# Kernel optimization log

Hardware: AMD Instinct MI355X
Metric: run time of the kernel (lower is better)

The kernel has to match this reference:

```python
import jax, jax.numpy as jnp
import numpy as np

B, D, L = 8, 512, 2000          # batch, encoder_out_dim, seq_len
E = 300                          # embedding_dim
N1, N2 = 118, 8929               # hierarchy level sizes


def setup_inputs() -> dict:
    key = jax.random.key(0)
    k = jax.random.split(key, 6)
    H = jax.random.normal(k[0], (B, D, L), dtype=jnp.float32)
    Q1w = jax.random.normal(k[1], (N1, E), dtype=jnp.float32) * 0.05   # cat_embedding_matrix
    Q2w = jax.random.normal(k[2], (N2, E), dtype=jnp.float32) * 0.05   # label_embedding_matrix
    # Q12: xavier_uniform over [N2, N1]
    bound = float(np.sqrt(6.0 / (N1 + N2)))
    Q12w = jax.random.uniform(k[3], (N2, N1), minval=-bound, maxval=bound, dtype=jnp.float32)
    # 1x1 conv mapping: weight [D, E], bias [D] (kernel_size=1 squeezed)
    cbound = float(np.sqrt(1.0 / E))
    Wmap = jax.random.uniform(k[4], (D, E), minval=-cbound, maxval=cbound, dtype=jnp.float32)
    bmap = jax.random.uniform(k[5], (D,), minval=-cbound, maxval=cbound, dtype=jnp.float32)
    return {"H": H, "Q1w": Q1w, "Q2w": Q2w, "Q12w": Q12w, "Wmap": Wmap, "bmap": bmap}


def reference(H, Q1w, Q2w, Q12w, Wmap, bmap):
    # 1x1 conv mapping == affine map over embedding dim: [n, E] @ [E, D] + b
    Q1 = Q1w @ Wmap.T + bmap                      # [N1, D]
    E1 = jnp.einsum('nd,bdl->bnl', Q1, H)         # level-1 scores [B, N1, L]
    A1 = jax.nn.softmax(E1, axis=2)
    C1 = jnp.einsum('bnl,bdl->bnd', A1, H)        # [B, N1, D]
    C1 = jnp.einsum('mn,bnd->bmd', Q12w, C1)      # project to level 2: [B, N2, D]
    Q2 = (Q2w @ Wmap.T + bmap) * C1               # [N2, D] * [B, N2, D]
    E2 = jnp.einsum('bmd,bdl->bml', Q2, H)        # level-2 scores [B, N2, L]
    A2 = jax.nn.softmax(E2, axis=2)
    C2 = jnp.einsum('bml,bdl->bmd', A2, H)        # [B, N2, D]
    return (C2, A2)
```

## Files before the change

### kernel.cpp

```cpp
#include <hip/hip_runtime.h>

typedef short    bf16x8 __attribute__((ext_vector_type(8)));
typedef float    f32x4  __attribute__((ext_vector_type(4)));
typedef unsigned short u16x8 __attribute__((ext_vector_type(8)));

__device__ __forceinline__ unsigned short f2bf(float f) {
    unsigned u = __float_as_uint(f);
    return (unsigned short)((u + 0x7fffu + ((u >> 16) & 1u)) >> 16);
}
__device__ __forceinline__ float bf2f(unsigned short h) {
    return __uint_as_float((unsigned)h << 16);
}

template<bool> struct otype            { using T = float; };
template<>     struct otype<true>      { using T = unsigned short; };

template<int BM,int BN,int TM,int TN,bool BT,bool VA,bool VB,bool OB>
__launch_bounds__(256)
__global__ void gemm_f32(const float* __restrict__ A, int lda, long long sA,
                         const float* __restrict__ B, int ldb, long long sB,
                         void* __restrict__ Cv, int ldc, long long sC,
                         int M, int N, int K,
                         const float* __restrict__ bias,
                         const float* __restrict__ mul, int mulld)
{
    constexpr int BK  = 16;
    constexpr int GSA = BM*4/TM;
    constexpr int GSB = BN*4/TN;
    __shared__ float As[BK][BM+4];
    __shared__ float Bs[BK][BN+4];

    const int bz = blockIdx.z;
    A += (long long)bz * sA;
    B += (long long)bz * sB;
    using OT = typename otype<OB>::T;
    OT* C = (OT*)Cv + (long long)bz * sC;
    const int m0 = blockIdx.y * BM;
    const int n0 = blockIdx.x * BN;
    const int tid = threadIdx.x;
    const int tm = tid >> 4;
    const int tn = tid & 15;

    float acc[TM][TN];
#pragma unroll
    for (int i=0;i<TM;++i)
#pragma unroll
        for (int j=0;j<TN;++j) acc[i][j]=0.f;

    for (int k0=0;k0<K;k0+=BK) {
        if constexpr (VA) {
#pragma unroll
            for (int r=0;r<BM*BK/1024;++r) {
                int v = tid + r*256;
                int m = v >> 2, k4 = (v & 3)*4;
                int gm = m0+m, gk = k0+k4;
                float4 val = make_float4(0.f,0.f,0.f,0.f);
                if (gm < M) {
                    if (gk+3 < K) {
                        val = *reinterpret_cast<const float4*>(A + (long long)gm*lda + gk);
                    } else {
                        float t0 = (gk   < K) ? A[(long long)gm*lda+gk  ] : 0.f;
                        float t1 = (gk+1 < K) ? A[(long long)gm*lda+gk+1] : 0.f;
                        float t2 = (gk+2 < K) ? A[(long long)gm*lda+gk+2] : 0.f;
                        val = make_float4(t0,t1,t2,0.f);
                    }
                }
                As[k4+0][m]=val.x; As[k4+1][m]=val.y; As[k4+2][m]=val.z; As[k4+3][m]=val.w;
            }
        } else {
#pragma unroll
            for (int r=0;r<BM*BK/256;++r) {
                int e = tid + r*256;
                int m = e >> 4, k = e & 15;
                int gm=m0+m, gk=k0+k;
                As[k][m] = (gm<M && gk<K) ? A[(long long)gm*lda+gk] : 0.f;
            }
        }
        if constexpr (!BT) {
            if constexpr (VB) {
#pragma unroll
                for (int r=0;r<BK*BN/1024;++r) {
                    int v = tid + r*256;
                    int k = v / (BN/4), n4 = (v % (BN/4))*4;
                    int gk=k0+k, gn=n0+n4;
                    float4 val = make_float4(0.f,0.f,0.f,0.f);
                    if (gk < K) {
                        if (gn+3 < N) {
                            val = *reinterpret_cast<const float4*>(B + (long long)gk*ldb + gn);
                        } else {
                            float t0=(gn  <N)?B[(long long)gk*ldb+gn  ]:0.f;
                            float t1=(gn+1<N)?B[(long long)gk*ldb+gn+1]:0.f;
                            float t2=(gn+2<N)?B[(long long)gk*ldb+gn+2]:0.f;
                            val = make_float4(t0,t1,t2,0.f);
                        }
                    }
                    Bs[k][n4+0]=val.x; Bs[k][n4+1]=val.y; Bs[k][n4+2]=val.z; Bs[k][n4+3]=val.w;
                }
            } else {
#pragma unroll
                for (int r=0;r<BK*BN/256;++r) {
                    int e = tid + r*256;
                    int k = e / BN, n = e % BN;
                    int gk=k0+k, gn=n0+n;
                    Bs[k][n] = (gk<K && gn<N) ? B[(long long)gk*ldb+gn] : 0.f;
                }
            }
        } else {
            if constexpr (VB) {
#pragma unroll
                for (int r=0;r<BN*BK/1024;++r) {
                    int v = tid + r*256;
                    int n = v >> 2, k4 = (v&3)*4;
                    int gn=n0+n, gk=k0+k4;
                    float4 val = make_float4(0.f,0.f,0.f,0.f);
                    if (gn < N) {
                        if (gk+3 < K) {
                            val = *reinterpret_cast<const float4*>(B + (long long)gn*ldb + gk);
                        } else {
                            float t0=(gk  <K)?B[(long long)gn*ldb+gk  ]:0.f;
                            float t1=(gk+1<K)?B[(long long)gn*ldb+gk+1]:0.f;
                            float t2=(gk+2<K)?B[(long long)gn*ldb+gk+2]:0.f;
                            val=make_float4(t0,t1,t2,0.f);
                        }
                    }
                    Bs[k4+0][n]=val.x; Bs[k4+1][n]=val.y; Bs[k4+2][n]=val.z; Bs[k4+3][n]=val.w;
                }
            } else {
#pragma unroll
                for (int r=0;r<BN*BK/256;++r) {
                    int e = tid + r*256;
                    int n = e >> 4, k = e & 15;
                    int gn=n0+n, gk=k0+k;
                    Bs[k][n] = (gn<N && gk<K) ? B[(long long)gn*ldb+gk] : 0.f;
                }
            }
        }
        __syncthreads();
#pragma unroll
        for (int kk=0;kk<BK;++kk) {
            float a[TM], bb[TN];
#pragma unroll
            for (int g=0;g<TM/4;++g) {
                float4 t = *reinterpret_cast<const float4*>(&As[kk][g*GSA + tm*4]);
                a[4*g+0]=t.x; a[4*g+1]=t.y; a[4*g+2]=t.z; a[4*g+3]=t.w;
            }
#pragma unroll
            for (int g=0;g<TN/4;++g) {
                float4 t = *reinterpret_cast<const float4*>(&Bs[kk][g*GSB + tn*4]);
                bb[4*g+0]=t.x; bb[4*g+1]=t.y; bb[4*g+2]=t.z; bb[4*g+3]=t.w;
            }
#pragma unroll
            for (int i=0;i<TM;++i)
#pragma unroll
                for (int j=0;j<TN;++j)
                    acc[i][j] = fmaf(a[i], bb[j], acc[i][j]);
        }
        __syncthreads();
    }
#pragma unroll
    for (int i=0;i<TM;++i) {
        int row = m0 + (i>>2)*GSA + tm*4 + (i&3);
        if (row < M) {
#pragma unroll
            for (int j=0;j<TN;++j) {
                int col = n0 + (j>>2)*GSB + tn*4 + (j&3);
                if (col < N) {
                    float val = acc[i][j];
                    if (bias) val += bias[col];
                    if (mul)  val *= mul[(long long)row*mulld + col];
                    if constexpr (OB) C[(long long)row*ldc + col] = f2bf(val);
                    else              C[(long long)row*ldc + col] = val;
                }
            }
        }
    }
}

template<unsigned F>
__launch_bounds__(512, 4)
__global__ void gemm_mfma_p(const unsigned short* __restrict__ A, int lda, long long sA,
                            const unsigned short* __restrict__ Bt, int ldb, long long sB,
                            void* __restrict__ Cv, int ldc, long long sC,
                            int M, int Ncols, int NX, int NY, int NT,
                            const float* __restrict__ bias,
                            const float* __restrict__ mul, int ldm,
                            float* __restrict__ partial, long long pstride,
                            const float* __restrict__ hsum,
                            const float* __restrict__ invs)
{
    __shared__ unsigned short lds[3][12288];

    const int nwg = gridDim.x;
    const int q = nwg >> 3, r = nwg & 7;
    const int xcd = blockIdx.x & 7, idx = blockIdx.x >> 3;
    const int wg = (xcd < r ? xcd*(q+1) : r*(q+1) + (xcd-r)*q) + idx;
    const int nx = wg % NX;
    const int t1 = wg / NX;
    const int my = t1 % NY;
    const int bz = t1 / NY;

    const int tid  = threadIdx.x;
    const int lane = tid & 63, wid = tid >> 6;
    const int wr = wid >> 2, wc = wid & 3;
    const int fr = lane & 15, fq = lane >> 4;
    const int m0 = my * 128;
    const int n0 = nx * 256;

    A  += (long long)bz * sA;
    Bt += (long long)bz * sB;

    const int srow = tid >> 2;
    const int scz  = (tid & 3) ^ ((srow >> 1) & 3);
    long long arow = m0 + srow; if (arow > M-1) arow = M-1;
    const unsigned short* aSrc  = A  + arow*lda + scz*8;
    const unsigned short* bSrc0 = Bt + (long long)(n0 + srow)*ldb + scz*8;
    const unsigned short* bSrc1 = bSrc0 + 128ll*ldb;

    int aoff[4], boff[4];
#pragma unroll
    for (int m=0;m<4;++m) {
        const int ra = wr*64 + m*16 + fr;
        aoff[m] = ra*64 + ((fq ^ ((ra>>1)&3))*16);
    }
#pragma unroll
    for (int n=0;n<4;++n) {
        const int rb = wc*64 + n*16 + fr;
        boff[n] = 8192 + rb*64 + ((fq ^ ((rb>>1)&3))*16);
    }

    f32x4 acc[4][4];
#pragma unroll
    for (int i=0;i<4;++i)
#pragma unroll
        for (int j=0;j<4;++j) acc[i][j] = (f32x4)(0.f);

    auto stage = [&](int s, int t) {
        const int koff = t*32;
        char* base = (char*)&lds[s][0];
        __builtin_amdgcn_global_load_lds(
            (const __attribute__((address_space(1))) void*)(aSrc + koff),
            (__attribute__((address_space(3))) void*)(base + tid*16), 16, 0, 0);
        __builtin_amdgcn_global_load_lds(
            (const __attribute__((address_space(1))) void*)(bSrc0 + koff),
            (__attribute__((address_space(3))) void*)(base + 8192 + tid*16), 16, 0, 0);
        __builtin_amdgcn_global_load_lds(
            (const __attribute__((address_space(1))) void*)(bSrc1 + koff),
            (__attribute__((address_space(3))) void*)(base + 16384 + tid*16), 16, 0, 0);
    };

    stage(0, 0);
    stage(1, NT > 1 ? 1 : 0);
    asm volatile("s_waitcnt vmcnt(3)" ::: "memory");
    __builtin_amdgcn_s_barrier();

    int cur = 0, stg = 2;
    for (int kt = 0; kt < NT; ++kt) {
        int tnx = kt + 2; if (tnx > NT-1) tnx = NT-1;
        stage(stg, tnx);
        const char* bp = (const char*)&lds[cur][0];
        bf16x8 a[4], b[4];
#pragma unroll
        for (int m=0;m<4;++m) a[m] = *(const bf16x8*)(bp + aoff[m]);
#pragma unroll
        for (int n=0;n<4;++n) b[n] = *(const bf16x8*)(bp + boff[n]);
        __builtin_amdgcn_s_setprio(1);
#pragma unroll
        for (int m=0;m<4;++m)
#pragma unroll
            for (int n=0;n<4;++n)
                acc[m][n] = __builtin_amdgcn_mfma_f32_16x16x32_bf16(a[m], b[n], acc[m][n], 0, 0, 0);
        __builtin_amdgcn_s_setprio(0);
        asm volatile("s_waitcnt lgkmcnt(0)" ::: "memory");
        asm volatile("s_waitcnt vmcnt(3)" ::: "memory");
        __builtin_amdgcn_s_barrier();
        cur = (cur == 2) ? 0 : cur + 1;
        stg = (stg == 2) ? 0 : stg + 1;
    }

    if constexpr ((F & 16) != 0) {
        __shared__ float sp[4][128];
        unsigned short* Cb = (unsigned short*)Cv + (long long)bz * sC;
        float rp[4][4];
#pragma unroll
        for (int m=0;m<4;++m)
#pragma unroll
            for (int j=0;j<4;++j) rp[m][j] = 0.f;
#pragma unroll
        for (int m=0;m<4;++m) {
            const int rb = m0 + wr*64 + m*16 + fq*4;
#pragma unroll
            for (int n=0;n<4;++n) {
                const int col = n0 + wc*64 + n*16 + fr;
#pragma unroll
                for (int j=0;j<4;++j) {
                    float x = __expf(acc[m][n][j]) - 1.0f;
                    rp[m][j] += x;
                    const int row = rb + j;
                    if (row < M) Cb[(long long)row*ldc + col] = f2bf(x);
                }
            }
        }
#pragma unroll
        for (int m=0;m<4;++m)
#pragma unroll
            for (int j=0;j<4;++j) {
                float s = rp[m][j];
                s += __shfl_xor(s, 1); s += __shfl_xor(s, 2);
                s += __shfl_xor(s, 4); s += __shfl_xor(s, 8);
                rp[m][j] = s;
            }
        if (fr == 0) {
#pragma unroll
            for (int m=0;m<4;++m)
#pragma unroll
                for (int j=0;j<4;++j)
                    sp[wc][wr*64 + m*16 + fq*4 + j] = rp[m][j];
        }
        __syncthreads();
        if (tid < 128) {
            const int row = m0 + tid;
            if (row < M) {
                float s = sp[0][tid] + sp[1][tid] + sp[2][tid] + sp[3][tid];
                partial[(long long)nx*pstride + (long long)bz*M + row] = s;
            }
        }
    } else if constexpr ((F & 8) != 0) {
        unsigned short* Ct = (unsigned short*)Cv + (long long)bz * sC;
#pragma unroll
        for (int m=0;m<4;++m) {
            const int rb = m0 + wr*64 + m*16 + fq*4;
#pragma unroll
            for (int n=0;n<4;++n) {
                const int col = n0 + wc*64 + n*16 + fr;
                if (col < Ncols) {
#pragma unroll
                    for (int j=0;j<4;++j) {
                        const int row = rb + j;
                        float val = (row < M) ? acc[m][n][j] : 0.f;
                        Ct[(long long)col*ldc + row] = f2bf(val);
                    }
                }
            }
        }
    } else {
        float*          Cf = (float*)Cv + (long long)bz * sC;
        unsigned short* Cb = (unsigned short*)Cv + (long long)bz * sC;
#pragma unroll
        for (int m=0;m<4;++m) {
            const int rb = m0 + wr*64 + m*16 + fq*4;
#pragma unroll
            for (int n=0;n<4;++n) {
                const int col = n0 + wc*64 + n*16 + fr;
                if (col < Ncols) {
                    float bv = 0.f, hv = 0.f;
                    if constexpr ((F & 1) != 0) bv = bias[col];
                    if constexpr ((F & 32) != 0) hv = hsum[(long long)bz*Ncols + col];
#pragma unroll
                    for (int j=0;j<4;++j) {
                        const int row = rb + j;
                        if (row < M) {
                            float val = acc[m][n][j];
                            if constexpr ((F & 1) != 0)  val += bv;
                            if constexpr ((F & 2) != 0)  val *= mul[(long long)row*ldm + col];
                            if constexpr ((F & 32) != 0) val = (val + hv) * invs[(long long)bz*M + row];
                            if constexpr ((F & 4) != 0)  Cb[(long long)row*ldc + col] = f2bf(val);
                            else                         Cf[(long long)row*ldc + col] = val;
                        }
                    }
                }
            }
        }
    }
}

template<bool AF32>
__launch_bounds__(512, 2)
__global__ void gemm_mfma(const void* __restrict__ Ain, int lda, long long sA,
                          const unsigned short* __restrict__ Bt, int ldb, long long sB,
                          float* __restrict__ C, int ldc, long long sC,
                          int M, int N, int K, int NT)
{
    __shared__ unsigned short As[2][128*32];
    __shared__ unsigned short Bs[2][256*32];

    const int tid  = threadIdx.x;
    const int lane = tid & 63, wid = tid >> 6;
    const int wr = wid >> 2, wc = wid & 3;
    const int fr = lane & 15, fq = lane >> 4;
    const int bz = blockIdx.z;
    const int m0 = blockIdx.y * 128;
    const int n0 = blockIdx.x * 256;

    const unsigned short* Ab = nullptr;
    const float*          Af = nullptr;
    if constexpr (AF32) Af = (const float*)Ain + (long long)bz * sA;
    else                Ab = (const unsigned short*)Ain + (long long)bz * sA;
    Bt += (long long)bz * sB;
    C  += (long long)bz * sC;

    const int srow = tid >> 2;
    const int sc   = tid & 3;
    const int scz  = sc ^ ((srow >> 1) & 3);
    int arow = m0 + srow; if (arow > M-1) arow = M-1;
    const bool am_ok = (m0 + srow) < M;
    const long long brow0 = n0 + srow;
    const long long brow1 = n0 + 128 + srow;
    const int ldsA  = wid << 10;
    const int ldsB0 = wid << 10;
    const int ldsB1 = 8192 + (wid << 10);

    f32x4 acc[4][4];
#pragma unroll
    for (int i=0;i<4;++i)
#pragma unroll
        for (int j=0;j<4;++j) acc[i][j] = (f32x4)(0.f);

    auto stage = [&](int buf, int t) {
        const long long koff = (long long)t * 32;
        __builtin_amdgcn_global_load_lds(
            (const __attribute__((address_space(1))) void*)(Bt + brow0*ldb + koff + scz*8),
            (__attribute__((address_space(3))) void*)((char*)&Bs[buf][0] + ldsB0), 16, 0, 0);
        __builtin_amdgcn_global_load_lds(
            (const __attribute__((address_space(1))) void*)(Bt + brow1*ldb + koff + scz*8),
            (__attribute__((address_space(3))) void*)((char*)&Bs[buf][0] + ldsB1), 16, 0, 0);
        if constexpr (!AF32) {
            __builtin_amdgcn_global_load_lds(
                (const __attribute__((address_space(1))) void*)(Ab + (long long)arow*lda + koff + scz*8),
                (__attribute__((address_space(3))) void*)((char*)&As[buf][0] + ldsA), 16, 0, 0);
        } else {
            const float* src = Af + (long long)arow*lda + koff + scz*8;
            const int kk = t*32 + scz*8;
            float4 z = make_float4(0.f,0.f,0.f,0.f);
            float4 v0 = (am_ok && kk   < K) ? *(const float4*)(src  ) : z;
            float4 v1 = (am_ok && kk+4 < K) ? *(const float4*)(src+4) : z;
            u16x8 o;
            o[0]=f2bf(v0.x); o[1]=f2bf(v0.y); o[2]=f2bf(v0.z); o[3]=f2bf(v0.w);
            o[4]=f2bf(v1.x); o[5]=f2bf(v1.y); o[6]=f2bf(v1.z); o[7]=f2bf(v1.w);
            *(u16x8*)((char*)&As[buf][0] + tid*16) = o;
        }
    };

    stage(0, 0);
    int cur = 0;
    for (int t = 0; t < NT; ++t) {
        __syncthreads();
        if (t + 1 < NT) stage(cur ^ 1, t + 1);
        const unsigned short* as = As[cur];
        const unsigned short* bs = Bs[cur];
        bf16x8 a[4], b[4];
#pragma unroll
        for (int m=0;m<4;++m) {
            const int ra = wr*64 + m*16 + fr;
            a[m] = *(const bf16x8*)(as + ra*32 + (fq ^ ((ra>>1)&3))*8);
        }
#pragma unroll
        for (int n=0;n<4;++n) {
            const int rb = wc*64 + n*16 + fr;
            b[n] = *(const bf16x8*)(bs + rb*32 + (fq ^ ((rb>>1)&3))*8);
        }
        __builtin_amdgcn_s_setprio(1);
#pragma unroll
        for (int m=0;m<4;++m)
#pragma unroll
            for (int n=0;n<4;++n)
                acc[m][n] = __builtin_amdgcn_mfma_f32_16x16x32_bf16(a[m], b[n], acc[m][n], 0, 0, 0);
        __builtin_amdgcn_s_setprio(0);
        cur ^= 1;
    }
#pragma unroll
    for (int m=0;m<4;++m) {
        const int rb = m0 + wr*64 + m*16 + fq*4;
#pragma unroll
        for (int n=0;n<4;++n) {
            const int col = n0 + wc*64 + n*16 + fr;
            if (col < N) {
#pragma unroll
                for (int j=0;j<4;++j) {
                    const int row = rb + j;
                    if (row < M) C[(long long)row*ldc + col] = acc[m][n][j];
                }
            }
        }
    }
}

__global__ __launch_bounds__(256) void cvt_pad_bf16(const float* __restrict__ H,
                                                    unsigned short* __restrict__ Hb)
{
    const long long idx = (long long)blockIdx.x * 256 + threadIdx.x;
    const long long row = idx >> 8;
    const int l0 = (int)(idx & 255) * 8;
    u16x8 o = (u16x8)(unsigned short)0;
    if (l0 + 8 <= 2000) {
        const float* s = H + row*2000 + l0;
        float4 v0 = *(const float4*)(s);
        float4 v1 = *(const float4*)(s+4);
        o[0]=f2bf(v0.x); o[1]=f2bf(v0.y); o[2]=f2bf(v0.z); o[3]=f2bf(v0.w);
        o[4]=f2bf(v1.x); o[5]=f2bf(v1.y); o[6]=f2bf(v1.z); o[7]=f2bf(v1.w);
    }
    *(u16x8*)(Hb + row*2048 + l0) = o;
}

__global__ __launch_bounds__(256) void cvt_transpose_bf16(const float* __restrict__ H,
                                                          unsigned short* __restrict__ Ht)
{
    __shared__ unsigned short T[64][80];
    const int bz = blockIdx.z;
    const int d0 = blockIdx.y * 64;
    const int l0 = blockIdx.x * 64;
    const float* Hsrc = H + ((long long)bz*512 + d0) * 2000;
    unsigned short* Hdst = Ht + ((long long)bz*2048 + l0) * 512 + d0;
    const int tid = threadIdx.x;
    const int dl = tid >> 2;
    const int lc = (tid & 3) * 16;
#pragma unroll
    for (int i=0;i<4;++i) {
        const int l = lc + i*4;
        const int gl = l0 + l;
        float4 v = make_float4(0.f,0.f,0.f,0.f);
        if (gl < 2000) v = *(const float4*)(Hsrc + (long long)dl*2000 + gl);
        T[l+0][dl] = f2bf(v.x);
        T[l+1][dl] = f2bf(v.y);
        T[l+2][dl] = f2bf(v.z);
        T[l+3][dl] = f2bf(v.w);
    }
    __syncthreads();
    const int ll = tid >> 2;
    const int dc = (tid & 3) * 16;
    u16x8 w0 = *(const u16x8*)&T[ll][dc];
    u16x8 w1 = *(const u16x8*)&T[ll][dc+8];
    *(u16x8*)(Hdst + (long long)ll*512 + dc    ) = w0;
    *(u16x8*)(Hdst + (long long)ll*512 + dc + 8) = w1;
}

__global__ __launch_bounds__(256) void cvt_rows_bf16(const float* __restrict__ src,
                                                     unsigned short* __restrict__ dst,
                                                     long long rows, int scols, int dcols)
{
    const long long i = (long long)blockIdx.x * 256 + threadIdx.x;
    if (i < rows * (long long)dcols) {
        const long long r = i / dcols;
        const int c = (int)(i - r*dcols);
        dst[i] = (c < scols) ? f2bf(src[r*scols + c]) : (unsigned short)0;
    }
}

__global__ __launch_bounds__(256) void hsum_k(const float* __restrict__ H,
                                              float* __restrict__ Hsum)
{
    const int row  = blockIdx.x*4 + (threadIdx.x >> 6);
    const int lane = threadIdx.x & 63;
    const float* h = H + (long long)row * 2000;
    float s = 0.f;
    for (int c = lane*4; c < 2000; c += 256) {
        float4 v = *(const float4*)(h + c);
        s += (v.x + v.y) + (v.z + v.w);
    }
#pragma unroll
    for (int o=32;o;o>>=1) s += __shfl_xor(s, o);
    if (lane == 0) Hsum[row] = s;
}

__global__ __launch_bounds__(256) void normalize_k(const unsigned short* __restrict__ A2b,
                                                   const float* __restrict__ partial,
                                                   long long pstride,
                                                   float* __restrict__ A2,
                                                   float* __restrict__ invs)
{
    const long long row = blockIdx.x;
    float s = 0.f;
#pragma unroll
    for (int i=0;i<8;++i) s += partial[i*pstride + row];
    const float inv = 1.0f / (2000.0f + s);
    if (threadIdx.x == 0) invs[row] = inv;
    const int tid = threadIdx.x;
    if (tid < 250) {
        u16x8 v = *(const u16x8*)(A2b + row*2048 + tid*8);
        float* a2 = A2 + row*2000 + tid*8;
        float4 o0, o1;
        o0.x = (1.0f + bf2f((unsigned short)v[0])) * inv;
        o0.y = (1.0f + bf2f((unsigned short)v[1])) * inv;
        o0.z = (1.0f + bf2f((unsigned short)v[2])) * inv;
        o0.w = (1.0f + bf2f((unsigned short)v[3])) * inv;
        o1.x = (1.0f + bf2f((unsigned short)v[4])) * inv;
        o1.y = (1.0f + bf2f((unsigned short)v[5])) * inv;
        o1.z = (1.0f + bf2f((unsigned short)v[6])) * inv;
        o1.w = (1.0f + bf2f((unsigned short)v[7])) * inv;
        *(float4*)(a2    ) = o0;
        *(float4*)(a2 + 4) = o1;
    }
}

__global__ __launch_bounds__(256) void softmax_rows(float* __restrict__ X, int L,
                                                    unsigned short* __restrict__ Xb, int Lb)
{
    const long long row = blockIdx.x;
    float* x = X + row * (long long)L;
    const int tid = threadIdx.x;
    const int nv = L >> 2;
    const bool h0 = tid < nv;
    const bool h1 = tid + 256 < nv;
    float4 t0 = make_float4(0.f,0.f,0.f,0.f);
    float4 t1 = make_float4(0.f,0.f,0.f,0.f);
    float mx = -3.402823e38f;
    if (h0) { t0 = *reinterpret_cast<const float4*>(x + 4*tid);
              mx = fmaxf(fmaxf(t0.x,t0.y), fmaxf(t0.z,t0.w)); }
    if (h1) { t1 = *reinterpret_cast<const float4*>(x + 4*(tid+256));
              mx = fmaxf(mx, fmaxf(fmaxf(t1.x,t1.y), fmaxf(t1.z,t1.w))); }
    __shared__ float sred[4];
#pragma unroll
    for (int o=32;o;o>>=1) mx = fmaxf(mx, __shfl_xor(mx, o));
    if ((tid & 63)==0) sred[tid>>6] = mx;
    __syncthreads();
    mx = fmaxf(fmaxf(sred[0],sred[1]), fmaxf(sred[2],sred[3]));
    __syncthreads();
    float s = 0.f;
    if (h0) {
        t0.x=__expf(t0.x-mx); t0.y=__expf(t0.y-mx); t0.z=__expf(t0.z-mx); t0.w=__expf(t0.w-mx);
        s += (t0.x+t0.y)+(t0.z+t0.w);
    }
    if (h1) {
        t1.x=__expf(t1.x-mx); t1.y=__expf(t1.y-mx); t1.z=__expf(t1.z-mx); t1.w=__expf(t1.w-mx);
        s += (t1.x+t1.y)+(t1.z+t1.w);
    }
#pragma unroll
    for (int o=32;o;o>>=1) s += __shfl_xor(s, o);
    if ((tid & 63)==0) sred[tid>>6] = s;
    __syncthreads();
    s = (sred[0]+sred[1])+(sred[2]+sred[3]);
    const float inv = 1.0f / s;
    if (h0) { t0.x*=inv; t0.y*=inv; t0.z*=inv; t0.w*=inv;
              *reinterpret_cast<float4*>(x + 4*tid) = t0; }
    if (h1) { t1.x*=inv; t1.y*=inv; t1.z*=inv; t1.w*=inv;
              *reinterpret_cast<float4*>(x + 4*(tid+256)) = t1; }
    if (Xb) {
        unsigned short* xb = Xb + row * (long long)Lb;
        if (h0) {
            ushort4 o; o.x=f2bf(t0.x); o.y=f2bf(t0.y); o.z=f2bf(t0.z); o.w=f2bf(t0.w);
            *reinterpret_cast<ushort4*>(xb + 4*tid) = o;
        }
        if (h1) {
            ushort4 o; o.x=f2bf(t1.x); o.y=f2bf(t1.y); o.z=f2bf(t1.z); o.w=f2bf(t1.w);
            *reinterpret_cast<ushort4*>(xb + 4*(tid+256)) = o;
        }
        if (tid < (Lb - L)/4) {
            ushort4 z; z.x=z.y=z.z=z.w=0;
            *reinterpret_cast<ushort4*>(xb + L + 4*tid) = z;
        }
    }
}

extern "C" void kernel_launch(void* const* d_in, const int* in_sizes, int n_in,
                              void* d_out, int out_size, void* d_ws, size_t ws_size,
                              hipStream_t stream)
{
    const float* H    = (const float*)d_in[0];
    const float* Q1w  = (const float*)d_in[1];
    const float* Q2w  = (const float*)d_in[2];
    const float* Q12w = (const float*)d_in[3];
    const float* Wmap = (const float*)d_in[4];
    const float* bmap = (const float*)d_in[5];

    constexpr long long B=8, D=512, L=2000, N1=118, N2=8929;
    constexpr long long C2E = B*N2*D;
    float* out = (float*)d_out;
    float* C2  = out;
    float* A2  = out + C2E;

    dim3 blk(256);

    size_t off = 0;
    auto alloc = [&](size_t n)->size_t { off = (off + 255) & ~(size_t)255; size_t o = off; off += n; return o; };
    const size_t oHb    = alloc(8ll*512*2048*2);
    const size_t oHtb   = alloc(8ll*2048*512*2);
    const size_t oWb    = alloc(512ll*320*2);
    const size_t oQ1wb  = alloc(118ll*320*2);
    const size_t oQ2wb  = alloc(8929ll*320*2);
    const size_t oQ12wb = alloc(8929ll*128*2);
    const size_t oQ1b   = alloc(118ll*512*2);
    const size_t oEmb   = alloc(8929ll*512*4);
    const size_t oE1    = alloc(8ll*118*2000*4);
    const size_t oA1b   = alloc(8ll*118*2048*2);
    const size_t oC1tb  = alloc(8ll*512*128*2);
    const size_t oQ2b   = alloc(8ll*8929*512*2);
    const size_t oA2b   = alloc(8ll*8929*2048*2);
    const size_t oPart  = alloc(8ll*8*8929*4);
    const size_t oInvs  = alloc(8ll*8929*4);
    const size_t oHsum  = alloc(8ll*512*4);
    const size_t FULL_NEED = off;

    char* ws = (char*)d_ws;

    if (ws_size >= FULL_NEED) {
        unsigned short* Hb    = (unsigned short*)(ws + oHb);
        unsigned short* Htb   = (unsigned short*)(ws + oHtb);
        unsigned short* Wb    = (unsigned short*)(ws + oWb);
        unsigned short* Q1wb  = (unsigned short*)(ws + oQ1wb);
        unsigned short* Q2wb  = (unsigned short*)(ws + oQ2wb);
        unsigned short* Q12wb = (unsigned short*)(ws + oQ12wb);
        unsigned short* Q1b   = (unsigned short*)(ws + oQ1b);
        float*          emb   = (float*)(ws + oEmb);
        float*          E1    = (float*)(ws + oE1);
        unsigned short* A1b   = (unsigned short*)(ws + oA1b);
        unsigned short* C1tb  = (unsigned short*)(ws + oC1tb);
        unsigned short* Q2b   = (unsigned short*)(ws + oQ2b);
        unsigned short* A2b   = (unsigned short*)(ws + oA2b);
        float*          part  = (float*)(ws + oPart);
        float*          invs  = (float*)(ws + oInvs);
        float*          Hsum  = (float*)(ws + oHsum);

        cvt_pad_bf16<<<dim3(4096), blk, 0, stream>>>(H, Hb);
        cvt_transpose_bf16<<<dim3(32,8,8), blk, 0, stream>>>(H, Htb);
        cvt_rows_bf16<<<dim3((512*320+255)/256), blk, 0, stream>>>(Wmap, Wb, 512, 300, 320);
        cvt_rows_bf16<<<dim3((118*320+255)/256), blk, 0, stream>>>(Q1w, Q1wb, 118, 300, 320);
        cvt_rows_bf16<<<dim3((8929*320+255)/256), blk, 0, stream>>>(Q2w, Q2wb, 8929, 300, 320);
        cvt_rows_bf16<<<dim3((8929*128+255)/256), blk, 0, stream>>>(Q12w, Q12wb, 8929, 118, 128);
        hsum_k<<<dim3(1024), blk, 0, stream>>>(H, Hsum);

        gemm_mfma_p<5><<<dim3(2), dim3(512), 0, stream>>>(
            Q1wb, 320, 0, Wb, 320, 0, Q1b, 512, 0, 118, 512, 2, 1, 10,
            bmap, nullptr, 0, nullptr, 0, nullptr, nullptr);
        gemm_mfma_p<1><<<dim3(140), dim3(512), 0, stream>>>(
            Q2wb, 320, 0, Wb, 320, 0, emb, 512, 0, 8929, 512, 2, 70, 10,
            bmap, nullptr, 0, nullptr, 0, nullptr, nullptr);
        gemm_mfma_p<0><<<dim3(64), dim3(512), 0, stream>>>(
            Q1b, 512, 0, Htb, 512, 2048*512, E1, 2000, N1*L, 118, 2000, 8, 1, 16,
            nullptr, nullptr, 0, nullptr, 0, nullptr, nullptr);
        softmax_rows<<<dim3((unsigned)(B*N1)), blk, 0, stream>>>(E1, 2000, A1b, 2048);
        gemm_mfma_p<12><<<dim3(16), dim3(512), 0, stream>>>(
            A1b, 2048, N1*2048, Hb, 2048, 512*2048, C1tb, 128, 512*128, 118, 512, 2, 1, 64,
            nullptr, nullptr, 0, nullptr, 0, nullptr, nullptr);
        gemm_mfma_p<6><<<dim3(1120), dim3(512), 0, stream>>>(
            Q12wb, 128, 0, C1tb, 128, 512*128, Q2b, 512, N2*D, 8929, 512, 2, 70, 4,
            nullptr, emb, 512, nullptr, 0, nullptr, nullptr);
        gemm_mfma_p<16><<<dim3(4480), dim3(512), 0, stream>>>(
            Q2b, 512, N2*D, Htb, 512, 2048*512, A2b, 2048, N2*2048, 8929, 2048, 8, 70, 16,
            nullptr, nullptr, 0, part, 8ll*8929, nullptr, nullptr);
        normalize_k<<<dim3((unsigned)(B*N2)), blk, 0, stream>>>(A2b, part, 8ll*8929, A2, invs);
        gemm_mfma_p<32><<<dim3(1120), dim3(512), 0, stream>>>(
            A2b, 2048, N2*2048, Hb, 2048, 512*2048, C2, 512, N2*D, 8929, 512, 2, 70, 64,
            nullptr, nullptr, 0, nullptr, 0, Hsum, invs);
        return;
    }

    float* Q1  = A2;
    float* emb = Q1  + N1*D;
    float* E1  = emb + N2*D;
    float* C1  = E1  + B*N1*L;

    gemm_f32<64,64,4,4,true,true,true,false><<<dim3(8,2,1), blk, 0, stream>>>(
        Q1w, 300, 0, Wmap, 300, 0, Q1, 512, 0, (int)N1, (int)D, 300, bmap, nullptr, 0);
    gemm_f32<64,64,4,4,true,true,true,false><<<dim3(8,140,1), blk, 0, stream>>>(
        Q2w, 300, 0, Wmap, 300, 0, emb, 512, 0, (int)N2, (int)D, 300, bmap, nullptr, 0);
    gemm_f32<64,64,4,4,false,true,true,false><<<dim3(32,2,8), blk, 0, stream>>>(
        Q1, 512, 0, H, 2000, D*L, E1, 2000, N1*L, (int)N1, (int)L, (int)D, nullptr, nullptr, 0);
    softmax_rows<<<dim3((unsigned)(B*N1)), blk, 0, stream>>>(E1, (int)L, nullptr, 0);
    gemm_f32<64,64,4,4,true,true,true,false><<<dim3(8,2,8), blk, 0, stream>>>(
        E1, 2000, N1*L, H, 2000, D*L, C1, 512, N1*D, (int)N1, (int)D, (int)L, nullptr, nullptr, 0);

    constexpr long long HBE = 8ll*512*2048;
    if (ws_size >= (size_t)(2*HBE*sizeof(unsigned short))) {
        unsigned short* Hb  = (unsigned short*)d_ws;
        unsigned short* Htb = Hb + HBE;
        cvt_pad_bf16<<<dim3(4096), blk, 0, stream>>>(H, Hb);
        cvt_transpose_bf16<<<dim3(32,8,8), blk, 0, stream>>>(H, Htb);
        unsigned short* Q2b = (unsigned short*)C2;
        gemm_f32<64,64,4,4,false,false,true,true><<<dim3(8,140,8), blk, 0, stream>>>(
            Q12w, 118, 0, C1, 512, N1*D, Q2b, 512, N2*D, (int)N2, (int)D, (int)N1, nullptr, emb, 512);
        gemm_mfma_p<0><<<dim3(4480), dim3(512), 0, stream>>>(
            Q2b, 512, N2*D, Htb, 512, 2048*512, A2, 2000, N2*L, (int)N2, (int)L, 8, 70, 16,
            nullptr, nullptr, 0, nullptr, 0, nullptr, nullptr);
        softmax_rows<<<dim3((unsigned)(B*N2)), blk, 0, stream>>>(A2, (int)L, nullptr, 0);
        gemm_mfma<true><<<dim3(2,70,8), dim3(512), 0, stream>>>(
            A2, 2000, N2*L, Hb, 2048, 512*2048, C2, 512, N2*D,
            (int)N2, (int)D, 2000, 63);
    } else {
        float* Q2 = C2;
        gemm_f32<64,64,4,4,false,false,true,false><<<dim3(8,140,8), blk, 0, stream>>>(
            Q12w, 118, 0, C1, 512, N1*D, Q2, 512, N2*D, (int)N2, (int)D, (int)N1, nullptr, emb, 512);
        gemm_f32<128,128,8,8,false,true,true,false><<<dim3(16,70,8), blk, 0, stream>>>(
            Q2, 512, N2*D, H, 2000, D*L, A2, 2000, N2*L, (int)N2, (int)L, (int)D, nullptr, nullptr, 0);
        softmax_rows<<<dim3((unsigned)(B*N2)), blk, 0, stream>>>(A2, (int)L, nullptr, 0);
        gemm_f32<128,128,8,8,true,true,true,false><<<dim3(4,70,8), blk, 0, stream>>>(
            A2, 2000, N2*L, H, 2000, D*L, C2, 512, N2*D, (int)N2, (int)D, (int)L, nullptr, nullptr, 0);
    }
}
```

Before: 830.8 us.

## Fuse A2 normalization into final GEMM and merge H preprocessing kernels

Removes the separate normalize_k pass. The final A2·H GEMM now writes the normalized fp32 A2 from its staged LDS tiles (blocks with nx==0 only), with a small invs_k kernel computing the reciprocal row sums first. It also merges the pad, transpose and row-sum passes over H into one prep_h kernel plus a tiny reduction, so H is read once instead of three times. In exchange the GEMM carries extra global stores and a looser vmcnt wait in half its blocks, which may unbalance work across blocks.

```diff
diff --git a/kernel.cpp b/kernel.cpp
--- a/kernel.cpp
+++ b/kernel.cpp
@@ -186,7 +186,9 @@
                             const float* __restrict__ mul, int ldm,
                             float* __restrict__ partial, long long pstride,
                             const float* __restrict__ hsum,
-                            const float* __restrict__ invs)
+                            const float* __restrict__ invs,
+                            float* __restrict__ a2out,
+                            float* __restrict__ dump)
 {
     __shared__ unsigned short lds[3][12288];
 
@@ -215,6 +217,21 @@
     const unsigned short* aSrc  = A  + arow*lda + scz*8;
     const unsigned short* bSrc0 = Bt + (long long)(n0 + srow)*ldb + scz*8;
     const unsigned short* bSrc1 = bSrc0 + 128ll*ldb;
+
+    bool wrblk = false, a2ok = false;
+    float invv = 0.f;
+    float* a2p = nullptr;
+    if constexpr ((F & 64) != 0) {
+        wrblk = (nx == 0);
+        if (wrblk) {
+            const int rrow = m0 + srow;
+            a2ok = rrow < M;
+            const long long ridx = (long long)bz*M + (a2ok ? rrow : M-1);
+            invv = invs[ridx];
+            asm volatile("" : "+v"(invv));
+            a2p = a2out + ridx*2000ll;
+        }
+    }
 
     int aoff[4], boff[4];
 #pragma unroll
@@ -270,8 +287,32 @@
             for (int n=0;n<4;++n)
                 acc[m][n] = __builtin_amdgcn_mfma_f32_16x16x32_bf16(a[m], b[n], acc[m][n], 0, 0, 0);
         __builtin_amdgcn_s_setprio(0);
+        if constexpr ((F & 64) != 0) {
+            if (wrblk) {
+                u16x8 av = *(const u16x8*)(bp + (tid << 4));
+                const int col0 = kt*32 + scz*8;
+                const bool ok = a2ok && (col0 < 2000);
+                float* p0 = ok ? (a2p + col0) : (dump + (tid << 3));
+                float4 o0, o1;
+                o0.x = fmaf(bf2f((unsigned short)av[0]), invv, invv);
+                o0.y = fmaf(bf2f((unsigned short)av[1]), invv, invv);
+                o0.z = fmaf(bf2f((unsigned short)av[2]), invv, invv);
+                o0.w = fmaf(bf2f((unsigned short)av[3]), invv, invv);
+                o1.x = fmaf(bf2f((unsigned short)av[4]), invv, invv);
+                o1.y = fmaf(bf2f((unsigned short)av[5]), invv, invv);
+                o1.z = fmaf(bf2f((unsigned short)av[6]), invv, invv);
+                o1.w = fmaf(bf2f((unsigned short)av[7]), invv, invv);
+                *(float4*)(p0    ) = o0;
+                *(float4*)(p0 + 4) = o1;
+            }
+        }
         asm volatile("s_waitcnt lgkmcnt(0)" ::: "memory");
-        asm volatile("s_waitcnt vmcnt(3)" ::: "memory");
+        if constexpr ((F & 64) != 0) {
+            if (wrblk) asm volatile("s_waitcnt vmcnt(5)" ::: "memory");
+            else       asm volatile("s_waitcnt vmcnt(3)" ::: "memory");
+        } else {
+            asm volatile("s_waitcnt vmcnt(3)" ::: "memory");
+        }
         __builtin_amdgcn_s_barrier();
         cur = (cur == 2) ? 0 : cur + 1;
         stg = (stg == 2) ? 0 : stg + 1;
@@ -484,6 +525,79 @@
     }
 }
 
+__global__ __launch_bounds__(256) void prep_h(const float* __restrict__ H,
+                                              unsigned short* __restrict__ Hb,
+                                              unsigned short* __restrict__ Htb,
+                                              float* __restrict__ hpart)
+{
+    __shared__ unsigned short T[64][80];
+    const int bz = blockIdx.z;
+    const int d0 = blockIdx.y * 64;
+    const int l0 = blockIdx.x * 64;
+    const float* Hsrc = H + ((long long)bz*512 + d0) * 2000;
+    const int tid = threadIdx.x;
+    const int dl = tid >> 2;
+    const int lc = (tid & 3) * 16;
+    float4 v[4];
+    float s = 0.f;
+#pragma unroll
+    for (int i=0;i<4;++i) {
+        const int gl = l0 + lc + i*4;
+        v[i] = make_float4(0.f,0.f,0.f,0.f);
+        if (gl < 2000) v[i] = *(const float4*)(Hsrc + (long long)dl*2000 + gl);
+        s += (v[i].x + v[i].y) + (v[i].z + v[i].w);
+        T[lc+i*4+0][dl] = f2bf(v[i].x);
+        T[lc+i*4+1][dl] = f2bf(v[i].y);
+        T[lc+i*4+2][dl] = f2bf(v[i].z);
+        T[lc+i*4+3][dl] = f2bf(v[i].w);
+    }
+    {
+        unsigned short* hb = Hb + ((long long)bz*512 + d0 + dl)*2048 + l0 + lc;
+        u16x8 h0, h1;
+        h0[0]=f2bf(v[0].x); h0[1]=f2bf(v[0].y); h0[2]=f2bf(v[0].z); h0[3]=f2bf(v[0].w);
+        h0[4]=f2bf(v[1].x); h0[5]=f2bf(v[1].y); h0[6]=f2bf(v[1].z); h0[7]=f2bf(v[1].w);
+        h1[0]=f2bf(v[2].x); h1[1]=f2bf(v[2].y); h1[2]=f2bf(v[2].z); h1[3]=f2bf(v[2].w);
+        h1[4]=f2bf(v[3].x); h1[5]=f2bf(v[3].y); h1[6]=f2bf(v[3].z); h1[7]=f2bf(v[3].w);
+        *(u16x8*)(hb    ) = h0;
+        *(u16x8*)(hb + 8) = h1;
+    }
+    s += __shfl_xor(s, 1);
+    s += __shfl_xor(s, 2);
+    if ((tid & 3) == 0)
+        hpart[(long long)blockIdx.x*4096 + bz*512 + d0 + dl] = s;
+    __syncthreads();
+    unsigned short* Hdst = Htb + ((long long)bz*2048 + l0) * 512 + d0;
+    const int ll = tid >> 2;
+    const int dc = (tid & 3) * 16;
+    u16x8 w0 = *(const u16x8*)&T[ll][dc];
+    u16x8 w1 = *(const u16x8*)&T[ll][dc+8];
+    *(u16x8*)(Hdst + (long long)ll*512 + dc    ) = w0;
+    *(u16x8*)(Hdst + (long long)ll*512 + dc + 8) = w1;
+}
+
+__global__ __launch_bounds__(256) void reduce_hsum(const float* __restrict__ hpart,
+                                                   float* __restrict__ Hsum)
+{
+    const int r = blockIdx.x*256 + threadIdx.x;
+    float s = 0.f;
+#pragma unroll
+    for (int i=0;i<32;++i) s += hpart[(long long)i*4096 + r];
+    Hsum[r] = s;
+}
+
+__global__ __launch_bounds__(256) void invs_k(const float* __restrict__ partial,
+                                              long long pstride,
+                                              float* __restrict__ invs, int n)
+{
+    const int r = blockIdx.x*256 + threadIdx.x;
+    if (r < n) {
+        float s = 0.f;
+#pragma unroll
+        for (int i=0;i<8;++i) s += partial[i*pstride + r];
+        invs[r] = 1.0f / (2000.0f + s);
+    }
+}
+
 __global__ __launch_bounds__(256) void cvt_pad_bf16(const float* __restrict__ H,
                                                     unsigned short* __restrict__ Hb)
 {
@@ -542,52 +656,6 @@
         const long long r = i / dcols;
         const int c = (int)(i - r*dcols);
         dst[i] = (c < scols) ? f2bf(src[r*scols + c]) : (unsigned short)0;
-    }
-}
-
-__global__ __launch_bounds__(256) void hsum_k(const float* __restrict__ H,
-                                              float* __restrict__ Hsum)
-{
-    const int row  = blockIdx.x*4 + (threadIdx.x >> 6);
-    const int lane = threadIdx.x & 63;
-    const float* h = H + (long long)row * 2000;
-    float s = 0.f;
-    for (int c = lane*4; c < 2000; c += 256) {
-        float4 v = *(const float4*)(h + c);
-        s += (v.x + v.y) + (v.z + v.w);
-    }
-#pragma unroll
-    for (int o=32;o;o>>=1) s += __shfl_xor(s, o);
-    if (lane == 0) Hsum[row] = s;
-}
-
-__global__ __launch_bounds__(256) void normalize_k(const unsigned short* __restrict__ A2b,
-                                                   const float* __restrict__ partial,
-                                                   long long pstride,
-                                                   float* __restrict__ A2,
-                                                   float* __restrict__ invs)
-{
-    const long long row = blockIdx.x;
-    float s = 0.f;
-#pragma unroll
-    for (int i=0;i<8;++i) s += partial[i*pstride + row];
-    const float inv = 1.0f / (2000.0f + s);
-    if (threadIdx.x == 0) invs[row] = inv;
-    const int tid = threadIdx.x;
-    if (tid < 250) {
-        u16x8 v = *(const u16x8*)(A2b + row*2048 + tid*8);
-        float* a2 = A2 + row*2000 + tid*8;
-        float4 o0, o1;
-        o0.x = (1.0f + bf2f((unsigned short)v[0])) * inv;
-        o0.y = (1.0f + bf2f((unsigned short)v[1])) * inv;
-        o0.z = (1.0f + bf2f((unsigned short)v[2])) * inv;
-        o0.w = (1.0f + bf2f((unsigned short)v[3])) * inv;
-        o1.x = (1.0f + bf2f((unsigned short)v[4])) * inv;
-        o1.y = (1.0f + bf2f((unsigned short)v[5])) * inv;
-        o1.z = (1.0f + bf2f((unsigned short)v[6])) * inv;
-        o1.w = (1.0f + bf2f((unsigned short)v[7])) * inv;
-        *(float4*)(a2    ) = o0;
-        *(float4*)(a2 + 4) = o1;
     }
 }
 
@@ -687,6 +755,7 @@
     const size_t oPart  = alloc(8ll*8*8929*4);
     const size_t oInvs  = alloc(8ll*8929*4);
     const size_t oHsum  = alloc(8ll*512*4);
+    const size_t oHpart = alloc(32ll*4096*4);
     const size_t FULL_NEED = off;
 
     char* ws = (char*)d_ws;
@@ -708,38 +777,38 @@
         float*          part  = (float*)(ws + oPart);
         float*          invs  = (float*)(ws + oInvs);
         float*          Hsum  = (float*)(ws + oHsum);
-
-        cvt_pad_bf16<<<dim3(4096), blk, 0, stream>>>(H, Hb);
-        cvt_transpose_bf16<<<dim3(32,8,8), blk, 0, stream>>>(H, Htb);
+        float*          hpart = (float*)(ws + oHpart);
+
+        prep_h<<<dim3(32,8,8), blk, 0, stream>>>(H, Hb, Htb, hpart);
+        reduce_hsum<<<dim3(16), blk, 0, stream>>>(hpart, Hsum);
         cvt_rows_bf16<<<dim3((512*320+255)/256), blk, 0, stream>>>(Wmap, Wb, 512, 300, 320);
         cvt_rows_bf16<<<dim3((118*320+255)/256), blk, 0, stream>>>(Q1w, Q1wb, 118, 300, 320);
         cvt_rows_bf16<<<dim3((8929*320+255)/256), blk, 0, stream>>>(Q2w, Q2wb, 8929, 300, 320);
         cvt_rows_bf16<<<dim3((8929*128+255)/256), blk, 0, stream>>>(Q12w, Q12wb, 8929, 118, 128);
-        hsum_k<<<dim3(1024), blk, 0, stream>>>(H, Hsum);
 
         gemm_mfma_p<5><<<dim3(2), dim3(512), 0, stream>>>(
             Q1wb, 320, 0, Wb, 320, 0, Q1b, 512, 0, 118, 512, 2, 1, 10,
-            bmap, nullptr, 0, nullptr, 0, nullptr, nullptr);
+            bmap, nullptr, 0, nullptr, 0, nullptr, nullptr, nullptr, nullptr);
         gemm_mfma_p<1><<<dim3(140), dim3(512), 0, stream>>>(
             Q2wb, 320, 0, Wb, 320, 0, emb, 512, 0, 8929, 512, 2, 70, 10,
-            bmap, nullptr, 0, nullptr, 0, nullptr, nullptr);
+            bmap, nullptr, 0, nullptr, 0, nullptr, nullptr, nullptr, nullptr);
         gemm_mfma_p<0><<<dim3(64), dim3(512), 0, stream>>>(
             Q1b, 512, 0, Htb, 512, 2048*512, E1, 2000, N1*L, 118, 2000, 8, 1, 16,
-            nullptr, nullptr, 0, nullptr, 0, nullptr, nullptr);
+            nullptr, nullptr, 0, nullptr, 0, nullptr, nullptr, nullptr, nullptr);
         softmax_rows<<<dim3((unsigned)(B*N1)), blk, 0, stream>>>(E1, 2000, A1b, 2048);
         gemm_mfma_p<12><<<dim3(16), dim3(512), 0, stream>>>(
             A1b, 2048, N1*2048, Hb, 2048, 512*2048, C1tb, 128, 512*128, 118, 512, 2, 1, 64,
-            nullptr, nullptr, 0, nullptr, 0, nullptr, nullptr);
+            nullptr, nullptr, 0, nullptr, 0, nullptr, nullptr, nullptr, nullptr);
         gemm_mfma_p<6><<<dim3(1120), dim3(512), 0, stream>>>(
             Q12wb, 128, 0, C1tb, 128, 512*128, Q2b, 512, N2*D, 8929, 512, 2, 70, 4,
-            nullptr, emb, 512, nullptr, 0, nullptr, nullptr);
+            nullptr, emb, 512, nullptr, 0, nullptr, nullptr, nullptr, nullptr);
         gemm_mfma_p<16><<<dim3(4480), dim3(512), 0, stream>>>(
             Q2b, 512, N2*D, Htb, 512, 2048*512, A2b, 2048, N2*2048, 8929, 2048, 8, 70, 16,
-            nullptr, nullptr, 0, part, 8ll*8929, nullptr, nullptr);
-        normalize_k<<<dim3((unsigned)(B*N2)), blk, 0, stream>>>(A2b, part, 8ll*8929, A2, invs);
-        gemm_mfma_p<32><<<dim3(1120), dim3(512), 0, stream>>>(
+            nullptr, nullptr, 0, part, 8ll*8929, nullptr, nullptr, nullptr, nullptr);
+        invs_k<<<dim3(280), blk, 0, stream>>>(part, 8ll*8929, invs, (int)(B*N2));
+        gemm_mfma_p<96><<<dim3(1120), dim3(512), 0, stream>>>(
             A2b, 2048, N2*2048, Hb, 2048, 512*2048, C2, 512, N2*D, 8929, 512, 2, 70, 64,
-            nullptr, nullptr, 0, nullptr, 0, Hsum, invs);
+            nullptr, nullptr, 0, nullptr, 0, Hsum, invs, A2, part);
         return;
     }
 
@@ -769,7 +838,7 @@
             Q12w, 118, 0, C1, 512, N1*D, Q2b, 512, N2*D, (int)N2, (int)D, (int)N1, nullptr, emb, 512);
         gemm_mfma_p<0><<<dim3(4480), dim3(512), 0, stream>>>(
             Q2b, 512, N2*D, Htb, 512, 2048*512, A2, 2000, N2*L, (int)N2, (int)L, 8, 70, 16,
-            nullptr, nullptr, 0, nullptr, 0, nullptr, nullptr);
+            nullptr, nullptr, 0, nullptr, 0, nullptr, nullptr, nullptr, nullptr);
         softmax_rows<<<dim3((unsigned)(B*N2)), blk, 0, stream>>>(A2, (int)L, nullptr, 0);
         gemm_mfma<true><<<dim3(2,70,8), dim3(512), 0, stream>>>(
             A2, 2000, N2*L, Hb, 2048, 512*2048, C2, 512, N2*D,
```

After: 810.4 us. -2.5%, faster.
